# Kernel optimization log

Measured on AMD Instinct MI355X. Metric: run time of the kernel, lower is better.

The kernel has to match this reference:

```python
import jax, jax.numpy as jnp
import numpy as np

EMBED_DIM = 1024
NUM_HEADS = 16
HEAD_DIM = EMBED_DIM // NUM_HEADS
EPS = 1e-5


def setup_inputs() -> dict:
    key = jax.random.key(0)
    ks = jax.random.split(key, 16)
    B, SQ, SK = 4, 1024, 2048
    s = 1.0 / np.sqrt(EMBED_DIM)
    inp = {
        "query": jax.random.normal(ks[0], (B, SQ, EMBED_DIM), jnp.float32),
        "key": jax.random.normal(ks[1], (B, SK, EMBED_DIM), jnp.float32),
        "value": jax.random.normal(ks[2], (B, SK, EMBED_DIM), jnp.float32),
        "Wq": jax.random.normal(ks[3], (EMBED_DIM, EMBED_DIM), jnp.float32) * s,
        "bq": jnp.zeros((EMBED_DIM,), jnp.float32),
        "Wk": jax.random.normal(ks[4], (EMBED_DIM, EMBED_DIM), jnp.float32) * s,
        "bk": jnp.zeros((EMBED_DIM,), jnp.float32),
        "Wv": jax.random.normal(ks[5], (EMBED_DIM, EMBED_DIM), jnp.float32) * s,
        "bv": jnp.zeros((EMBED_DIM,), jnp.float32),
        "Wo": jax.random.normal(ks[6], (EMBED_DIM, EMBED_DIM), jnp.float32) * s,
        "bo": jnp.zeros((EMBED_DIM,), jnp.float32),
        "gamma": jnp.ones((EMBED_DIM,), jnp.float32),
        "beta": jnp.zeros((EMBED_DIM,), jnp.float32),
    }
    return inp


def reference(query, key, value, Wq, bq, Wk, bk, Wv, bv, Wo, bo, gamma, beta):
    B, SQ, E = query.shape
    SK = key.shape[1]
    residual = query
    # projections (nn.Linear: x @ W.T + b)
    Q = (query @ Wq.T + bq).reshape(B, SQ, NUM_HEADS, HEAD_DIM).transpose(0, 2, 1, 3)
    K = (key @ Wk.T + bk).reshape(B, SK, NUM_HEADS, HEAD_DIM).transpose(0, 2, 1, 3)
    V = (value @ Wv.T + bv).reshape(B, SK, NUM_HEADS, HEAD_DIM).transpose(0, 2, 1, 3)
    # scaled dot-product attention (mask=None, dropout in eval mode = identity)
    scores = jnp.einsum('bhqd,bhkd->bhqk', Q, K) / np.sqrt(HEAD_DIM).astype(np.float32)
    attn = jax.nn.softmax(scores, axis=-1)
    ctx = jnp.einsum('bhqk,bhkd->bhqd', attn, V)  # [B,H,SQ,D]
    ctx = ctx.transpose(0, 2, 1, 3).reshape(B, SQ, E)
    out = ctx @ Wo.T + bo
    # residual + LayerNorm
    x = out + residual
    mu = jnp.mean(x, axis=-1, keepdims=True)
    var = jnp.mean(jnp.square(x - mu), axis=-1, keepdims=True)
    return (x - mu) / jnp.sqrt(var + EPS) * gamma + beta
```

## Files before the change

### kernel.cpp

```cpp
#include <hip/hip_runtime.h>

#define NH   16
#define HD   64
#define SQL  1024
#define SKL  2048
#define EMB  1024

typedef __bf16 bf16x8 __attribute__((ext_vector_type(8)));
typedef float  f32x4  __attribute__((ext_vector_type(4)));

#define LOG2E 1.44269504088896f

__device__ __forceinline__ unsigned short f2bf(float f) {
  unsigned u = __builtin_bit_cast(unsigned, f);
  u += 0x7FFFu + ((u >> 16) & 1u);
  return (unsigned short)(u >> 16);
}
__device__ __forceinline__ __bf16 f2bf16(float f) {
  return __builtin_bit_cast(__bf16, f2bf(f));
}

typedef __attribute__((address_space(1))) void gvoid_t;
typedef __attribute__((address_space(3))) void lvoid_t;

__device__ __forceinline__ void async_copy16(const void* g, void* l) {
  __builtin_amdgcn_global_load_lds((gvoid_t*)g, (lvoid_t*)l, 16, 0, 0);
}

__global__ void cvt3_k(const float* __restrict__ q, const float* __restrict__ k,
                       const float* __restrict__ v, unsigned short* __restrict__ qb,
                       unsigned short* __restrict__ kb, unsigned short* __restrict__ vb)
{
  const int seg = blockIdx.y;
  const float* src = (seg == 0) ? q : ((seg == 1) ? k : v);
  unsigned short* dst = (seg == 0) ? qb : ((seg == 1) ? kb : vb);
  const int n8 = (seg == 0) ? (4 * 1024 * 1024 / 8) : (8 * 1024 * 1024 / 8);
  const int i = blockIdx.x * 256 + threadIdx.x;
  if (i >= n8) return;
  const float4 a  = ((const float4*)src)[2 * (size_t)i];
  const float4 b2 = ((const float4*)src)[2 * (size_t)i + 1];
  uint4 o;
  o.x = f2bf(a.x)  | ((unsigned)f2bf(a.y)  << 16);
  o.y = f2bf(a.z)  | ((unsigned)f2bf(a.w)  << 16);
  o.z = f2bf(b2.x) | ((unsigned)f2bf(b2.y) << 16);
  o.w = f2bf(b2.z) | ((unsigned)f2bf(b2.w) << 16);
  ((uint4*)dst)[i] = o;
}

__global__ void cvtw_k(const float* __restrict__ w0, const float* __restrict__ w1,
                       const float* __restrict__ w2, const float* __restrict__ w3,
                       unsigned short* __restrict__ out)
{
  const int seg = blockIdx.y;
  const float* src = (seg == 0) ? w0 : ((seg == 1) ? w1 : ((seg == 2) ? w2 : w3));
  unsigned short* dst = out + (size_t)seg * 1024 * 1024;
  const int i = blockIdx.x * 256 + threadIdx.x;
  const float4 a  = ((const float4*)src)[2 * (size_t)i];
  const float4 b2 = ((const float4*)src)[2 * (size_t)i + 1];
  uint4 o;
  o.x = f2bf(a.x)  | ((unsigned)f2bf(a.y)  << 16);
  o.y = f2bf(a.z)  | ((unsigned)f2bf(a.w)  << 16);
  o.z = f2bf(b2.x) | ((unsigned)f2bf(b2.y) << 16);
  o.w = f2bf(b2.z) | ((unsigned)f2bf(b2.w) << 16);
  ((uint4*)dst)[i] = o;
}

template<int MODE>
__device__ __forceinline__
void gemm_body(unsigned short* sA, unsigned short* sB,
               const unsigned short* __restrict__ A, const unsigned short* __restrict__ Bw,
               const float* __restrict__ bias, void* __restrict__ Cout,
               const float* __restrict__ resid, int Slog, float scale, int bm, int bn)
{
  const int tid = threadIdx.x;
  const int lane = tid & 63, w = tid >> 6;
  const int g = lane >> 4, lr = lane & 15;
  const int wm = w >> 1, wn = w & 1;

  f32x4 acc[4][4] = {};

  for (int k0 = 0; k0 < 1024; k0 += 64) {
#pragma unroll
    for (int i = 0; i < 4; ++i) {
      const int chunk = (i * 4 + w) * 64 + lane;
      const int o = chunk * 16;
      const int row = o >> 7;
      const int c2 = (o & 127) >> 1;
      async_copy16(A  + (size_t)(bm + row) * 1024 + k0 + c2, sA + (i * 4 + w) * 512);
      async_copy16(Bw + (size_t)(bn + row) * 1024 + k0 + c2, sB + (i * 4 + w) * 512);
    }
    __syncthreads();
#pragma unroll
    for (int kc = 0; kc < 2; ++kc) {
      const int kb = kc * 64 + g * 16;
      bf16x8 af[4], bf[4];
#pragma unroll
      for (int mi = 0; mi < 4; ++mi) {
        const int r = wm * 64 + mi * 16 + lr;
        af[mi] = *(const bf16x8*)((const char*)sA + ((r << 7) | kb));
      }
#pragma unroll
      for (int ni = 0; ni < 4; ++ni) {
        const int r = wn * 64 + ni * 16 + lr;
        bf[ni] = *(const bf16x8*)((const char*)sB + ((r << 7) | kb));
      }
#pragma unroll
      for (int mi = 0; mi < 4; ++mi)
#pragma unroll
        for (int ni = 0; ni < 4; ++ni)
          acc[mi][ni] = __builtin_amdgcn_mfma_f32_16x16x32_bf16(af[mi], bf[ni], acc[mi][ni], 0, 0, 0);
    }
    __syncthreads();
  }

  if (MODE == 0) {
    unsigned short* O = (unsigned short*)Cout;
    const int S = 1 << Slog;
#pragma unroll
    for (int ni = 0; ni < 4; ++ni) {
      const int col = bn + wn * 64 + ni * 16 + lr;
      const float bv = bias[col];
      const int hh = col >> 6, d = col & 63;
#pragma unroll
      for (int mi = 0; mi < 4; ++mi) {
#pragma unroll
        for (int j = 0; j < 4; ++j) {
          const int row = bm + wm * 64 + mi * 16 + g * 4 + j;
          const int bI = row >> Slog, s2 = row & (S - 1);
          O[(((size_t)(bI * NH + hh)) * S + s2) * HD + d] = f2bf((acc[mi][ni][j] + bv) * scale);
        }
      }
    }
  } else {
    float* O = (float*)Cout;
#pragma unroll
    for (int ni = 0; ni < 4; ++ni) {
      const int col = bn + wn * 64 + ni * 16 + lr;
      const float bv = bias[col];
#pragma unroll
      for (int mi = 0; mi < 4; ++mi) {
#pragma unroll
        for (int j = 0; j < 4; ++j) {
          const int row = bm + wm * 64 + mi * 16 + g * 4 + j;
          const size_t idx = (size_t)row * 1024 + col;
          O[idx] = acc[mi][ni][j] + bv + resid[idx];
        }
      }
    }
  }
}

__global__ __launch_bounds__(256, 2)
void proj3_k(const unsigned short* __restrict__ qb, const unsigned short* __restrict__ kb,
             const unsigned short* __restrict__ vb, const unsigned short* __restrict__ Wb,
             const float* __restrict__ bq, const float* __restrict__ bk,
             const float* __restrict__ bv, unsigned short* __restrict__ Qp,
             unsigned short* __restrict__ Kp, unsigned short* __restrict__ Vp)
{
  __shared__ __attribute__((aligned(16))) unsigned short sA[128 * 64];
  __shared__ __attribute__((aligned(16))) unsigned short sB[128 * 64];
  const int seg = blockIdx.z;
  if (seg == 0 && blockIdx.x >= 32) return;
  const unsigned short* A   = (seg == 0) ? qb : ((seg == 1) ? kb : vb);
  const unsigned short* W   = Wb + ((size_t)seg << 20);
  const float*          bia = (seg == 0) ? bq : ((seg == 1) ? bk : bv);
  unsigned short*       O   = (seg == 0) ? Qp : ((seg == 1) ? Kp : Vp);
  const int   Slog  = (seg == 0) ? 10 : 11;
  const float scale = (seg == 0) ? 0.125f : 1.0f;
  gemm_body<0>(sA, sB, A, W, bia, O, nullptr, Slog, scale, blockIdx.x * 128, blockIdx.y * 128);
}

__global__ __launch_bounds__(256, 2)
void gemm_o_k(const unsigned short* __restrict__ ctx, const unsigned short* __restrict__ Wo,
              const float* __restrict__ bo, float* __restrict__ xb,
              const float* __restrict__ resid)
{
  __shared__ __attribute__((aligned(16))) unsigned short sA[128 * 64];
  __shared__ __attribute__((aligned(16))) unsigned short sB[128 * 64];
  gemm_body<1>(sA, sB, ctx, Wo, bo, xb, resid, 10, 1.0f, blockIdx.x * 128, blockIdx.y * 128);
}

__global__ __launch_bounds__(256, 2)
void attn_k(const unsigned short* __restrict__ Qp, const unsigned short* __restrict__ Kp,
            const unsigned short* __restrict__ Vp, unsigned short* __restrict__ ctx)
{
  __shared__ __attribute__((aligned(16))) unsigned short sK[128 * 64];
  __shared__ __attribute__((aligned(16))) __bf16 sVt[64 * 136];
  __shared__ __attribute__((aligned(16))) __bf16 sP[4][32 * 136];

  const int tid = threadIdx.x, lane = tid & 63, w = tid >> 6;
  const int g = lane >> 4, lr = lane & 15;
  const int b = blockIdx.z, h = blockIdx.y;
  const int q0 = blockIdx.x * 128 + w * 32;
  const size_t qbase  = ((size_t)(b * NH + h)) * SQL * HD;
  const size_t kvbase = ((size_t)(b * NH + h)) * SKL * HD;

  bf16x8 aq[2][2];
#pragma unroll
  for (int mi = 0; mi < 2; ++mi)
#pragma unroll
    for (int kc = 0; kc < 2; ++kc)
      aq[mi][kc] = *(const bf16x8*)(Qp + qbase + (size_t)(q0 + mi * 16 + lr) * HD + kc * 32 + g * 8);

  f32x4 c[2][4] = {};
  float mrun[2][4], lrun[2][4];
#pragma unroll
  for (int mi = 0; mi < 2; ++mi)
#pragma unroll
    for (int j = 0; j < 4; ++j) { mrun[mi][j] = -__builtin_inff(); lrun[mi][j] = 0.f; }

  for (int kt = 0; kt < SKL / 128; ++kt) {
#pragma unroll
    for (int i = 0; i < 4; ++i) {
      const int chunk = (i * 4 + w) * 64 + lane;
      const int o = chunk * 16;
      const int row = o >> 7;
      const int colb = (o & 127) ^ ((row & 7) << 4);
      async_copy16(Kp + kvbase + (size_t)(kt * 128 + row) * HD + (colb >> 1),
                   sK + (i * 4 + w) * 512);
    }
#pragma unroll
    for (int i = 0; i < 4; ++i) {
      const int chunk = i * 256 + tid;
      const int k = chunk & 127, dblk = chunk >> 7;
      bf16x8 v = *(const bf16x8*)(Vp + kvbase + (size_t)(kt * 128 + k) * HD + dblk * 8);
#pragma unroll
      for (int j = 0; j < 8; ++j)
        sVt[(dblk * 8 + j) * 136 + k] = v[j];
    }
    __syncthreads();

    f32x4 s[2][8] = {};
#pragma unroll
    for (int kc = 0; kc < 2; ++kc) {
      const int kb = kc * 64 + g * 16;
#pragma unroll
      for (int ni = 0; ni < 8; ++ni) {
        const int r = ni * 16 + lr;
        bf16x8 bk = *(const bf16x8*)((const char*)sK + ((r << 7) | (kb ^ ((r & 7) << 4))));
        s[0][ni] = __builtin_amdgcn_mfma_f32_16x16x32_bf16(aq[0][kc], bk, s[0][ni], 0, 0, 0);
        s[1][ni] = __builtin_amdgcn_mfma_f32_16x16x32_bf16(aq[1][kc], bk, s[1][ni], 0, 0, 0);
      }
    }

#pragma unroll
    for (int mi = 0; mi < 2; ++mi) {
#pragma unroll
      for (int j = 0; j < 4; ++j) {
        float rm = s[mi][0][j];
#pragma unroll
        for (int ni = 1; ni < 8; ++ni) rm = fmaxf(rm, s[mi][ni][j]);
#pragma unroll
        for (int off = 1; off < 16; off <<= 1) rm = fmaxf(rm, __shfl_xor(rm, off));
        const float mnew = fmaxf(mrun[mi][j], rm);
        const float sc = __builtin_exp2f((mrun[mi][j] - mnew) * LOG2E);
        mrun[mi][j] = mnew;
#pragma unroll
        for (int nd = 0; nd < 4; ++nd) c[mi][nd][j] *= sc;
        float rs = 0.f;
#pragma unroll
        for (int ni = 0; ni < 8; ++ni) {
          const float p = __builtin_exp2f((s[mi][ni][j] - mnew) * LOG2E);
          rs += p;
          sP[w][(mi * 16 + g * 4 + j) * 136 + ni * 16 + lr] = f2bf16(p);
        }
#pragma unroll
        for (int off = 1; off < 16; off <<= 1) rs += __shfl_xor(rs, off);
        lrun[mi][j] = lrun[mi][j] * sc + rs;
      }
    }
    __syncthreads();

#pragma unroll
    for (int kc = 0; kc < 4; ++kc) {
      const int ko = kc * 32 + g * 8;
      bf16x8 pa[2];
#pragma unroll
      for (int mi = 0; mi < 2; ++mi)
        pa[mi] = *(const bf16x8*)(&sP[w][(mi * 16 + lr) * 136 + ko]);
#pragma unroll
      for (int nd = 0; nd < 4; ++nd) {
        bf16x8 vf = *(const bf16x8*)(&sVt[(nd * 16 + lr) * 136 + ko]);
        c[0][nd] = __builtin_amdgcn_mfma_f32_16x16x32_bf16(pa[0], vf, c[0][nd], 0, 0, 0);
        c[1][nd] = __builtin_amdgcn_mfma_f32_16x16x32_bf16(pa[1], vf, c[1][nd], 0, 0, 0);
      }
    }
    __syncthreads();
  }

#pragma unroll
  for (int mi = 0; mi < 2; ++mi)
#pragma unroll
    for (int j = 0; j < 4; ++j) {
      const float inv = 1.0f / lrun[mi][j];
      const int qrow = q0 + mi * 16 + g * 4 + j;
#pragma unroll
      for (int nd = 0; nd < 4; ++nd) {
        const int d = nd * 16 + lr;
        ctx[((size_t)b * SQL + qrow) * EMB + h * HD + d] = f2bf(c[mi][nd][j] * inv);
      }
    }
}

__global__ __launch_bounds__(256)
void ln_k(const float* __restrict__ x, const float* __restrict__ gm,
          const float* __restrict__ bt, float* __restrict__ out)
{
  const int row = blockIdx.x, t = threadIdx.x;
  const float4 v = ((const float4*)(x + (size_t)row * 1024))[t];
  float s  = v.x + v.y + v.z + v.w;
  float ss = v.x * v.x + v.y * v.y + v.z * v.z + v.w * v.w;
#pragma unroll
  for (int off = 32; off > 0; off >>= 1) {
    s  += __shfl_xor(s, off);
    ss += __shfl_xor(ss, off);
  }
  __shared__ float red[8];
  const int wv = t >> 6, lane = t & 63;
  if (lane == 0) { red[wv] = s; red[4 + wv] = ss; }
  __syncthreads();
  s  = red[0] + red[1] + red[2] + red[3];
  ss = red[4] + red[5] + red[6] + red[7];
  const float mu  = s * (1.0f / 1024.0f);
  const float var = ss * (1.0f / 1024.0f) - mu * mu;
  const float r = rsqrtf(var + 1e-5f);
  const float4 gg = ((const float4*)gm)[t];
  const float4 bb = ((const float4*)bt)[t];
  float4 o;
  o.x = (v.x - mu) * r * gg.x + bb.x;
  o.y = (v.y - mu) * r * gg.y + bb.y;
  o.z = (v.z - mu) * r * gg.z + bb.z;
  o.w = (v.w - mu) * r * gg.w + bb.w;
  ((float4*)(out + (size_t)row * 1024))[t] = o;
}

extern "C" void kernel_launch(void* const* d_in, const int* in_sizes, int n_in,
                              void* d_out, int out_size, void* d_ws, size_t ws_size,
                              hipStream_t stream)
{
  (void)in_sizes; (void)n_in; (void)out_size; (void)ws_size;
  const float* query = (const float*)d_in[0];
  const float* key   = (const float*)d_in[1];
  const float* value = (const float*)d_in[2];
  const float* Wq = (const float*)d_in[3];
  const float* bq = (const float*)d_in[4];
  const float* Wk = (const float*)d_in[5];
  const float* bk = (const float*)d_in[6];
  const float* Wv = (const float*)d_in[7];
  const float* bv = (const float*)d_in[8];
  const float* Wo = (const float*)d_in[9];
  const float* bo = (const float*)d_in[10];
  const float* gamma = (const float*)d_in[11];
  const float* beta  = (const float*)d_in[12];

  char* ws = (char*)d_ws;
  unsigned short* Wb  = (unsigned short*)(ws);
  unsigned short* qb  = (unsigned short*)(ws + (8ull  << 20));
  unsigned short* ctx = qb;
  unsigned short* kb  = (unsigned short*)(ws + (16ull << 20));
  float*          xb  = (float*)         (ws + (16ull << 20));
  unsigned short* vb  = (unsigned short*)(ws + (32ull << 20));
  unsigned short* Qp  = (unsigned short*)(ws + (48ull << 20));
  unsigned short* Kp  = (unsigned short*)(ws + (56ull << 20));
  unsigned short* Vp  = (unsigned short*)(ws + (72ull << 20));

  cvt3_k<<<dim3(4096, 3), 256, 0, stream>>>(query, key, value, qb, kb, vb);
  cvtw_k<<<dim3(512, 4),  256, 0, stream>>>(Wq, Wk, Wv, Wo, Wb);
  proj3_k<<<dim3(64, 8, 3), 256, 0, stream>>>(qb, kb, vb, Wb, bq, bk, bv, Qp, Kp, Vp);
  attn_k<<<dim3(8, NH, 4), 256, 0, stream>>>(Qp, Kp, Vp, ctx);
  gemm_o_k<<<dim3(32, 8), 256, 0, stream>>>(ctx, Wb + (3u << 20), bo, xb, query);
  ln_k<<<dim3(4096), 256, 0, stream>>>(xb, gamma, beta, (float*)d_out);
}
```

Before: 395.4 us.

## Register-prefetch next K/V tile in attention, remap blocks per XCD, change LDS stride

The attention kernel now loads the next K/V tile from global memory into registers while computing on the current one, replacing the per-iteration async LDS copy and synchronous V load. The grid becomes 1D, and each block index is remapped so that all query blocks of one batch-head land on the same XCD, which improves L2 reuse of K/V. The LDS row stride for P and V-transpose drops from 136 to 132. This costs extra VGPRs for the prefetch buffers, which may reduce occupancy, and the new stride may change bank-conflict behaviour.

```diff
diff --git a/kernel.cpp b/kernel.cpp
--- a/kernel.cpp
+++ b/kernel.cpp
@@ -10,6 +10,7 @@
 typedef float  f32x4  __attribute__((ext_vector_type(4)));
 
 #define LOG2E 1.44269504088896f
+#define PSTR  132
 
 __device__ __forceinline__ unsigned short f2bf(float f) {
   unsigned u = __builtin_bit_cast(unsigned, f);
@@ -185,13 +186,18 @@
             const unsigned short* __restrict__ Vp, unsigned short* __restrict__ ctx)
 {
   __shared__ __attribute__((aligned(16))) unsigned short sK[128 * 64];
-  __shared__ __attribute__((aligned(16))) __bf16 sVt[64 * 136];
-  __shared__ __attribute__((aligned(16))) __bf16 sP[4][32 * 136];
+  __shared__ __attribute__((aligned(16))) __bf16 sVt[64 * PSTR];
+  __shared__ __attribute__((aligned(16))) __bf16 sP[4][32 * PSTR];
 
   const int tid = threadIdx.x, lane = tid & 63, w = tid >> 6;
   const int g = lane >> 4, lr = lane & 15;
-  const int b = blockIdx.z, h = blockIdx.y;
-  const int q0 = blockIdx.x * 128 + w * 32;
+
+  const int id  = blockIdx.x;
+  const int xcd = id & 7, t = id >> 3;
+  const int bh  = xcd * 8 + (t >> 3);
+  const int qb  = t & 7;
+  const int b = bh >> 4, h = bh & 15;
+  const int q0 = qb * 128 + w * 32;
   const size_t qbase  = ((size_t)(b * NH + h)) * SQL * HD;
   const size_t kvbase = ((size_t)(b * NH + h)) * SKL * HD;
 
@@ -209,26 +215,40 @@
 #pragma unroll
     for (int j = 0; j < 4; ++j) { mrun[mi][j] = -__builtin_inff(); lrun[mi][j] = 0.f; }
 
+  bf16x8 kA[4], vA[4];
+#pragma unroll
+  for (int i = 0; i < 4; ++i) {
+    const int c = i * 256 + tid;
+    kA[i] = *(const bf16x8*)(Kp + kvbase + (size_t)c * 8);
+    vA[i] = *(const bf16x8*)(Vp + kvbase + (size_t)(c & 127) * HD + (c >> 7) * 8);
+  }
+
   for (int kt = 0; kt < SKL / 128; ++kt) {
 #pragma unroll
     for (int i = 0; i < 4; ++i) {
-      const int chunk = (i * 4 + w) * 64 + lane;
-      const int o = chunk * 16;
-      const int row = o >> 7;
-      const int colb = (o & 127) ^ ((row & 7) << 4);
-      async_copy16(Kp + kvbase + (size_t)(kt * 128 + row) * HD + (colb >> 1),
-                   sK + (i * 4 + w) * 512);
+      const int cc = i * 256 + tid;
+      const int row = cc >> 3, cb = (cc & 7) * 16;
+      *(bf16x8*)((char*)sK + ((row << 7) | (cb ^ ((row & 7) << 4)))) = kA[i];
     }
 #pragma unroll
     for (int i = 0; i < 4; ++i) {
-      const int chunk = i * 256 + tid;
-      const int k = chunk & 127, dblk = chunk >> 7;
-      bf16x8 v = *(const bf16x8*)(Vp + kvbase + (size_t)(kt * 128 + k) * HD + dblk * 8);
+      const int cc = i * 256 + tid;
+      const int k = cc & 127, dblk = cc >> 7;
 #pragma unroll
       for (int j = 0; j < 8; ++j)
-        sVt[(dblk * 8 + j) * 136 + k] = v[j];
-    }
-    __syncthreads();
+        sVt[(dblk * 8 + j) * PSTR + k] = vA[i][j];
+    }
+    __syncthreads();
+
+    if (kt + 1 < SKL / 128) {
+      const size_t nb = kvbase + (size_t)(kt + 1) * 128 * HD;
+#pragma unroll
+      for (int i = 0; i < 4; ++i) {
+        const int cc = i * 256 + tid;
+        kA[i] = *(const bf16x8*)(Kp + nb + (size_t)cc * 8);
+        vA[i] = *(const bf16x8*)(Vp + nb + (size_t)(cc & 127) * HD + (cc >> 7) * 8);
+      }
+    }
 
     f32x4 s[2][8] = {};
 #pragma unroll
@@ -262,7 +282,7 @@
         for (int ni = 0; ni < 8; ++ni) {
           const float p = __builtin_exp2f((s[mi][ni][j] - mnew) * LOG2E);
           rs += p;
-          sP[w][(mi * 16 + g * 4 + j) * 136 + ni * 16 + lr] = f2bf16(p);
+          sP[w][(mi * 16 + g * 4 + j) * PSTR + ni * 16 + lr] = f2bf16(p);
         }
 #pragma unroll
         for (int off = 1; off < 16; off <<= 1) rs += __shfl_xor(rs, off);
@@ -277,10 +297,10 @@
       bf16x8 pa[2];
 #pragma unroll
       for (int mi = 0; mi < 2; ++mi)
-        pa[mi] = *(const bf16x8*)(&sP[w][(mi * 16 + lr) * 136 + ko]);
+        pa[mi] = *(const bf16x8*)(&sP[w][(mi * 16 + lr) * PSTR + ko]);
 #pragma unroll
       for (int nd = 0; nd < 4; ++nd) {
-        bf16x8 vf = *(const bf16x8*)(&sVt[(nd * 16 + lr) * 136 + ko]);
+        bf16x8 vf = *(const bf16x8*)(&sVt[(nd * 16 + lr) * PSTR + ko]);
         c[0][nd] = __builtin_amdgcn_mfma_f32_16x16x32_bf16(pa[0], vf, c[0][nd], 0, 0, 0);
         c[1][nd] = __builtin_amdgcn_mfma_f32_16x16x32_bf16(pa[1], vf, c[1][nd], 0, 0, 0);
       }
@@ -367,7 +387,7 @@
   cvt3_k<<<dim3(4096, 3), 256, 0, stream>>>(query, key, value, qb, kb, vb);
   cvtw_k<<<dim3(512, 4),  256, 0, stream>>>(Wq, Wk, Wv, Wo, Wb);
   proj3_k<<<dim3(64, 8, 3), 256, 0, stream>>>(qb, kb, vb, Wb, bq, bk, bv, Qp, Kp, Vp);
-  attn_k<<<dim3(8, NH, 4), 256, 0, stream>>>(Qp, Kp, Vp, ctx);
+  attn_k<<<dim3(512), 256, 0, stream>>>(Qp, Kp, Vp, ctx);
   gemm_o_k<<<dim3(32, 8), 256, 0, stream>>>(ctx, Wb + (3u << 20), bo, xb, query);
   ln_k<<<dim3(4096), 256, 0, stream>>>(xb, gamma, beta, (float*)d_out);
 }
```

New measurement: 343.7 us. -13.1%, faster.
